# Performance work log

Hardware: AMD Instinct MI355X
Metric: run time of the kernel (lower is better)

The kernel has to match this reference:

```python
import jax, jax.numpy as jnp
import numpy as np

N = 100000      # nodes
E = 1600000     # edges (avg degree 16)
NX = 3          # input feature dim (data.x.shape[1])
K = 2           # number of kernels (len(kernel_DD) = manifold dim)
ORDER = 2       # par['order']
DEPTH = 2       # par['depth']
EPS = 1e-12     # F.normalize eps


def setup_inputs() -> dict:
    key = jax.random.key(0)
    ks = jax.random.split(key, 10)
    x = jax.random.normal(ks[0], (N, NX), dtype=jnp.float32)
    # per-edge kernel weights for the k directional kernels (sparse N x N ops)
    K_DD_vals = 0.1 * jax.random.normal(ks[1], (K, E), dtype=jnp.float32)
    K_DA_vals = 0.1 * jax.random.normal(ks[2], (K, E), dtype=jnp.float32)
    # lin[0]: in = 18*k = 36, out = 72
    lin0_w = 0.05 * jax.random.normal(ks[3], (36, 72), dtype=jnp.float32)
    lin0_b = jnp.zeros((72,), dtype=jnp.float32)
    # MLP: 144 -> 128 -> 64
    mlp_w1 = 0.05 * jax.random.normal(ks[4], (144, 128), dtype=jnp.float32)
    mlp_b1 = jnp.zeros((128,), dtype=jnp.float32)
    mlp_w2 = 0.05 * jax.random.normal(ks[5], (128, 64), dtype=jnp.float32)
    mlp_b2 = jnp.zeros((64,), dtype=jnp.float32)
    src = jax.random.randint(ks[6], (E,), 0, N, dtype=jnp.int32)
    dst = jnp.sort(jax.random.randint(ks[7], (E,), 0, N, dtype=jnp.int32))
    return {"x": x, "K_DD_vals": K_DD_vals, "K_DA_vals": K_DA_vals,
            "lin0_w": lin0_w, "lin0_b": lin0_b,
            "mlp_w1": mlp_w1, "mlp_b1": mlp_b1,
            "mlp_w2": mlp_w2, "mlp_b2": mlp_b2,
            "src": src, "dst": dst}


def _aniso_conv(h, src, dst, k_vals):
    """Kernel-weighted message passing: out_j[t] = sum_{e: dst[e]=t} K_j[e] * h[src[e]].
    Concatenate the k kernel outputs along the channel dim ([N, C] -> [N, k*C])."""
    msgs = h[src]  # [E, C] gather (shared across kernels)
    outs = [jax.ops.segment_sum(k_vals[j][:, None] * msgs, dst, num_segments=N)
            for j in range(k_vals.shape[0])]
    return jnp.concatenate(outs, axis=1)


def reference(x, K_DD_vals, K_DA_vals, lin0_w, lin0_b,
              mlp_w1, mlp_b1, mlp_w2, mlp_b2, src, dst):
    # --- DD phase (order hops), collecting per-hop outputs ---
    h = x
    collected = []
    for _ in range(ORDER):
        h = _aniso_conv(h, src, dst, K_DD_vals)   # channels *= K each hop
        collected.append(h)
    h = jnp.concatenate(collected, axis=1)        # [N, NX*(K + K^2)] = [N, 18]

    # --- DA phase (depth hops) with Linear+ReLU between hops ---
    for i in range(DEPTH):
        h = _aniso_conv(h, src, dst, K_DA_vals)
        if i < DEPTH - 1:
            h = jax.nn.relu(h @ lin0_w + lin0_b)  # 36 -> 72

    # --- MLP head: 144 -> 128 -> 64 ---
    h = jax.nn.relu(h @ mlp_w1 + mlp_b1)
    h = h @ mlp_w2 + mlp_b2

    # --- L2 normalize (F.normalize, p=2, dim=-1) ---
    norm = jnp.maximum(jnp.linalg.norm(h, axis=-1, keepdims=True), EPS)
    return h / norm
```

## Files before the change

kernel.cpp:

```cpp
#include <hip/hip_runtime.h>

#define N_NODES 100000
#define N_EDGES 1600000

typedef __attribute__((ext_vector_type(8))) short short8;
typedef __attribute__((ext_vector_type(4))) float f32x4;
typedef __attribute__((ext_vector_type(2))) unsigned short ushort2v;
typedef __attribute__((ext_vector_type(4))) unsigned short ushort4v;
typedef __attribute__((ext_vector_type(8))) unsigned short ushort8v;

static __device__ inline unsigned short f2bf(float f) {
    union { float f; unsigned u; } v; v.f = f;
    unsigned r = v.u + 0x7FFF + ((v.u >> 16) & 1);
    return (unsigned short)(r >> 16);
}
static __device__ inline float bf2f(unsigned short u) {
    union { unsigned u; float f; } v; v.u = ((unsigned)u) << 16;
    return v.f;
}

__global__ __launch_bounds__(256) void rowptr_k(const int* __restrict__ dst,
                                                int* __restrict__ rp) {
    int t = blockIdx.x * blockDim.x + threadIdx.x;
    if (t > N_NODES) return;
    int lo = 0, hi = N_EDGES;
    while (lo < hi) {
        int mid = (lo + hi) >> 1;
        if (dst[mid] < t) lo = mid + 1; else hi = mid;
    }
    rp[t] = lo;
}

__global__ __launch_bounds__(256) void prep_k(const float* __restrict__ w1,
                                              const float* __restrict__ w2,
                                              const float* __restrict__ l0w,
                                              unsigned short* __restrict__ w1t,
                                              unsigned short* __restrict__ w2t,
                                              unsigned short* __restrict__ w0t) {
    int id = blockIdx.x * blockDim.x + threadIdx.x;
    if (id < 128 * 160) {
        int o = id / 160, k = id - o * 160;
        w1t[id] = (k < 144) ? f2bf(w1[k * 128 + o]) : (unsigned short)0;
    } else if (id < 128 * 160 + 64 * 128) {
        int j = id - 128 * 160;
        int o = j / 128, k = j - o * 128;
        w2t[j] = f2bf(w2[k * 64 + o]);
    } else if (id < 128 * 160 + 64 * 128 + 80 * 64) {
        int j = id - 128 * 160 - 64 * 128;
        int o = j / 64, k = j - o * 64;
        w0t[j] = (o < 72 && k < 36) ? f2bf(l0w[k * 72 + o]) : (unsigned short)0;
    }
}

template<int VEC> struct VecU;
template<> struct VecU<1> { using T = unsigned short; };
template<> struct VecU<2> { using T = ushort2v; };
template<> struct VecU<4> { using T = ushort4v; };
template<> struct VecU<8> { using T = ushort8v; };

template<int OUT_STRIDE>
__global__ __launch_bounds__(256) void conv1_k(const float* __restrict__ hin,
                                               const float* __restrict__ kv,
                                               const int* __restrict__ src,
                                               const int* __restrict__ rp,
                                               unsigned short* __restrict__ hout) {
    int id = blockIdx.x * blockDim.x + threadIdx.x;
    if (id >= N_NODES * 3) return;
    int t = id / 3;
    int c = id - t * 3;
    int e0 = rp[t], e1 = rp[t + 1];
    float a0 = 0.f, a1 = 0.f;
    int e = e0;
    for (; e + 4 <= e1; e += 4) {
        int s[4]; float k0[4], k1[4], v[4];
#pragma unroll
        for (int u = 0; u < 4; ++u) s[u]  = src[e + u];
#pragma unroll
        for (int u = 0; u < 4; ++u) k0[u] = kv[e + u];
#pragma unroll
        for (int u = 0; u < 4; ++u) k1[u] = kv[N_EDGES + e + u];
#pragma unroll
        for (int u = 0; u < 4; ++u) v[u]  = hin[(size_t)s[u] * 3 + c];
#pragma unroll
        for (int u = 0; u < 4; ++u) { a0 += k0[u] * v[u]; a1 += k1[u] * v[u]; }
    }
    for (; e < e1; ++e) {
        int s = src[e];
        float v = hin[(size_t)s * 3 + c];
        a0 += kv[e] * v;
        a1 += kv[N_EDGES + e] * v;
    }
    hout[(size_t)t * OUT_STRIDE + c]     = f2bf(a0);
    hout[(size_t)t * OUT_STRIDE + 3 + c] = f2bf(a1);
}

template<int C, int VEC, int IN_STRIDE, int OUT_STRIDE, int OUT_OFF,
         int PAD_FROM, int PAD_TO>
__global__ __launch_bounds__(256) void convb_k(const unsigned short* __restrict__ hin,
                                               const float* __restrict__ kv,
                                               const int* __restrict__ src,
                                               const int* __restrict__ rp,
                                               unsigned short* __restrict__ hout) {
    constexpr int G = C / VEC;
    using VT = typename VecU<VEC>::T;
    int id = blockIdx.x * blockDim.x + threadIdx.x;
    if (id >= N_NODES * G) return;
    int t = id / G;
    int g = id - t * G;
    int c0 = g * VEC;
    int e0 = rp[t], e1 = rp[t + 1];

    float a0[VEC], a1[VEC];
#pragma unroll
    for (int q = 0; q < VEC; ++q) { a0[q] = 0.f; a1[q] = 0.f; }

    int e = e0;
    for (; e + 4 <= e1; e += 4) {
        int s[4]; float k0[4], k1[4];
#pragma unroll
        for (int u = 0; u < 4; ++u) s[u]  = src[e + u];
#pragma unroll
        for (int u = 0; u < 4; ++u) k0[u] = kv[e + u];
#pragma unroll
        for (int u = 0; u < 4; ++u) k1[u] = kv[N_EDGES + e + u];
        VT v[4];
#pragma unroll
        for (int u = 0; u < 4; ++u)
            v[u] = *reinterpret_cast<const VT*>(hin + (size_t)s[u] * IN_STRIDE + c0);
#pragma unroll
        for (int u = 0; u < 4; ++u) {
            const unsigned short* vf = reinterpret_cast<const unsigned short*>(&v[u]);
#pragma unroll
            for (int q = 0; q < VEC; ++q) {
                float x = bf2f(vf[q]);
                a0[q] += k0[u] * x;
                a1[q] += k1[u] * x;
            }
        }
    }
    for (; e < e1; ++e) {
        int s = src[e];
        float k0 = kv[e], k1 = kv[N_EDGES + e];
        VT v = *reinterpret_cast<const VT*>(hin + (size_t)s * IN_STRIDE + c0);
        const unsigned short* vf = reinterpret_cast<const unsigned short*>(&v);
#pragma unroll
        for (int q = 0; q < VEC; ++q) {
            float x = bf2f(vf[q]);
            a0[q] += k0 * x;
            a1[q] += k1 * x;
        }
    }

    VT r0, r1;
    unsigned short* r0f = reinterpret_cast<unsigned short*>(&r0);
    unsigned short* r1f = reinterpret_cast<unsigned short*>(&r1);
#pragma unroll
    for (int q = 0; q < VEC; ++q) { r0f[q] = f2bf(a0[q]); r1f[q] = f2bf(a1[q]); }
    *reinterpret_cast<VT*>(hout + (size_t)t * OUT_STRIDE + OUT_OFF + c0)     = r0;
    *reinterpret_cast<VT*>(hout + (size_t)t * OUT_STRIDE + OUT_OFF + C + c0) = r1;

    if constexpr (PAD_TO > PAD_FROM) {
        if (g == G - 1) {
            ushort4v z = {0, 0, 0, 0};
#pragma unroll
            for (int j = PAD_FROM; j < PAD_TO; j += 4)
                *reinterpret_cast<ushort4v*>(hout + (size_t)t * OUT_STRIDE + j) = z;
        }
    }
}

__global__ __launch_bounds__(256) void lin0m_k(const unsigned short* __restrict__ h3b,
                                               const unsigned short* __restrict__ w0t,
                                               const float* __restrict__ b0,
                                               unsigned short* __restrict__ h4b) {
    int tid = threadIdx.x;
    int w = tid >> 6;
    int lane = tid & 63;
    int lr = lane & 15;
    int kg = lane >> 4;
    int row_base = blockIdx.x * 64 + w * 16;

    f32x4 acc[5];
#pragma unroll
    for (int n = 0; n < 5; ++n) acc[n] = (f32x4){0.f, 0.f, 0.f, 0.f};

    const unsigned short* arow = h3b + (size_t)(row_base + lr) * 64 + kg * 8;
#pragma unroll
    for (int ks = 0; ks < 2; ++ks) {
        short8 a = *reinterpret_cast<const short8*>(arow + ks * 32);
#pragma unroll
        for (int n = 0; n < 5; ++n) {
            short8 b = *reinterpret_cast<const short8*>(w0t + (n * 16 + lr) * 64 + ks * 32 + kg * 8);
            acc[n] = __builtin_amdgcn_mfma_f32_16x16x32_bf16(a, b, acc[n], 0, 0, 0);
        }
    }
#pragma unroll
    for (int n = 0; n < 5; ++n) {
        int col = n * 16 + lr;
        if (col < 72) {
            float bv = b0[col];
#pragma unroll
            for (int q = 0; q < 4; ++q) {
                int t = row_base + kg * 4 + q;
                if (t < N_NODES)
                    h4b[(size_t)t * 72 + col] = f2bf(fmaxf(acc[n][q] + bv, 0.f));
            }
        }
    }
}

#define HSTRIDE 136
__global__ __launch_bounds__(256) void mlp_k(const unsigned short* __restrict__ h5b,
                                             const unsigned short* __restrict__ w1t,
                                             const float* __restrict__ b1,
                                             const unsigned short* __restrict__ w2t,
                                             const float* __restrict__ b2,
                                             float* __restrict__ out) {
    __shared__ unsigned short sh[64 * HSTRIDE];
    int tid = threadIdx.x;
    int w = tid >> 6;
    int lane = tid & 63;
    int lr = lane & 15;
    int kg = lane >> 4;
    int row_base = blockIdx.x * 64 + w * 16;

    f32x4 acc[8];
#pragma unroll
    for (int n = 0; n < 8; ++n) acc[n] = (f32x4){0.f, 0.f, 0.f, 0.f};

    const unsigned short* arow = h5b + (size_t)(row_base + lr) * 160 + kg * 8;
#pragma unroll
    for (int ks = 0; ks < 5; ++ks) {
        short8 a = *reinterpret_cast<const short8*>(arow + ks * 32);
#pragma unroll
        for (int n = 0; n < 8; ++n) {
            short8 b = *reinterpret_cast<const short8*>(w1t + (n * 16 + lr) * 160 + ks * 32 + kg * 8);
            acc[n] = __builtin_amdgcn_mfma_f32_16x16x32_bf16(a, b, acc[n], 0, 0, 0);
        }
    }
#pragma unroll
    for (int n = 0; n < 8; ++n) {
        float bv = b1[n * 16 + lr];
#pragma unroll
        for (int q = 0; q < 4; ++q) {
            float hv = fmaxf(acc[n][q] + bv, 0.f);
            sh[(w * 16 + kg * 4 + q) * HSTRIDE + n * 16 + lr] = f2bf(hv);
        }
    }
    __syncthreads();

    f32x4 acc2[4];
#pragma unroll
    for (int n = 0; n < 4; ++n) acc2[n] = (f32x4){0.f, 0.f, 0.f, 0.f};
#pragma unroll
    for (int ks = 0; ks < 4; ++ks) {
        short8 a = *reinterpret_cast<const short8*>(sh + (w * 16 + lr) * HSTRIDE + ks * 32 + kg * 8);
#pragma unroll
        for (int n = 0; n < 4; ++n) {
            short8 b = *reinterpret_cast<const short8*>(w2t + (n * 16 + lr) * 128 + ks * 32 + kg * 8);
            acc2[n] = __builtin_amdgcn_mfma_f32_16x16x32_bf16(a, b, acc2[n], 0, 0, 0);
        }
    }

    float v[4][4];
    float ss[4];
#pragma unroll
    for (int q = 0; q < 4; ++q) ss[q] = 0.f;
#pragma unroll
    for (int n = 0; n < 4; ++n) {
        float bv = b2[n * 16 + lr];
#pragma unroll
        for (int q = 0; q < 4; ++q) {
            float x = acc2[n][q] + bv;
            v[n][q] = x;
            ss[q] += x * x;
        }
    }
#pragma unroll
    for (int q = 0; q < 4; ++q) {
#pragma unroll
        for (int d = 1; d < 16; d <<= 1) ss[q] += __shfl_xor(ss[q], d);
    }
#pragma unroll
    for (int q = 0; q < 4; ++q) {
        int node = row_base + kg * 4 + q;
        if (node < N_NODES) {
            float scale = 1.f / fmaxf(sqrtf(ss[q]), 1e-12f);
#pragma unroll
            for (int n = 0; n < 4; ++n)
                out[(size_t)node * 64 + n * 16 + lr] = v[n][q] * scale;
        }
    }
}

extern "C" void kernel_launch(void* const* d_in, const int* in_sizes, int n_in,
                              void* d_out, int out_size, void* d_ws, size_t ws_size,
                              hipStream_t stream) {
    const float* x   = (const float*)d_in[0];
    const float* kdd = (const float*)d_in[1];
    const float* kda = (const float*)d_in[2];
    const float* l0w = (const float*)d_in[3];
    const float* l0b = (const float*)d_in[4];
    const float* w1  = (const float*)d_in[5];
    const float* b1  = (const float*)d_in[6];
    const float* w2  = (const float*)d_in[7];
    const float* b2  = (const float*)d_in[8];
    const int*   src = (const int*)d_in[9];
    const int*   dst = (const int*)d_in[10];
    float* out = (float*)d_out;
    char* ws = (char*)d_ws;

    int*   rp  = (int*)ws;
    unsigned short* w0t = (unsigned short*)(ws + 400384u);
    unsigned short* w1t = (unsigned short*)(ws + 410624u);
    unsigned short* w2t = (unsigned short*)(ws + 451584u);
    unsigned short* hcb = (unsigned short*)(ws + 475136u);
    unsigned short* h3b = (unsigned short*)(ws + 4480000u);
    unsigned short* h4b = (unsigned short*)(ws + 17284096u);
    unsigned short* h5b = (unsigned short*)(ws + 31684096u);

    rowptr_k<<<(N_NODES + 1 + 255) / 256, 256, 0, stream>>>(dst, rp);
    prep_k<<<(128 * 160 + 64 * 128 + 80 * 64 + 255) / 256, 256, 0, stream>>>(w1, w2, l0w, w1t, w2t, w0t);

    conv1_k<20><<<(N_NODES * 3 + 255) / 256, 256, 0, stream>>>(x, kdd, src, rp, hcb);
    convb_k<6, 2, 20, 20, 6, 0, 0><<<(N_NODES * 3 + 255) / 256, 256, 0, stream>>>(hcb, kdd, src, rp, hcb);

    convb_k<18, 2, 20, 64, 0, 36, 64><<<(N_NODES * 9 + 255) / 256, 256, 0, stream>>>(hcb, kda, src, rp, h3b);
    lin0m_k<<<(N_NODES + 63) / 64, 256, 0, stream>>>(h3b, w0t, l0b, h4b);
    convb_k<72, 8, 72, 160, 0, 144, 160><<<(N_NODES * 9 + 255) / 256, 256, 0, stream>>>(h4b, kda, src, rp, h5b);

    mlp_k<<<(N_NODES + 63) / 64, 256, 0, stream>>>(h5b, w1t, b1, w2t, b2, out);
}
```

Before: 197.5 us.

## Fuse last DA conv into MLP head via shared memory; unroll edge loops by 8

```diff
diff --git a/kernel.cpp b/kernel.cpp
--- a/kernel.cpp
+++ b/kernel.cpp
@@ -71,18 +71,18 @@
     int e0 = rp[t], e1 = rp[t + 1];
     float a0 = 0.f, a1 = 0.f;
     int e = e0;
-    for (; e + 4 <= e1; e += 4) {
-        int s[4]; float k0[4], k1[4], v[4];
-#pragma unroll
-        for (int u = 0; u < 4; ++u) s[u]  = src[e + u];
-#pragma unroll
-        for (int u = 0; u < 4; ++u) k0[u] = kv[e + u];
-#pragma unroll
-        for (int u = 0; u < 4; ++u) k1[u] = kv[N_EDGES + e + u];
-#pragma unroll
-        for (int u = 0; u < 4; ++u) v[u]  = hin[(size_t)s[u] * 3 + c];
-#pragma unroll
-        for (int u = 0; u < 4; ++u) { a0 += k0[u] * v[u]; a1 += k1[u] * v[u]; }
+    for (; e + 8 <= e1; e += 8) {
+        int s[8]; float k0[8], k1[8], v[8];
+#pragma unroll
+        for (int u = 0; u < 8; ++u) s[u]  = src[e + u];
+#pragma unroll
+        for (int u = 0; u < 8; ++u) k0[u] = kv[e + u];
+#pragma unroll
+        for (int u = 0; u < 8; ++u) k1[u] = kv[N_EDGES + e + u];
+#pragma unroll
+        for (int u = 0; u < 8; ++u) v[u]  = hin[(size_t)s[u] * 3 + c];
+#pragma unroll
+        for (int u = 0; u < 8; ++u) { a0 += k0[u] * v[u]; a1 += k1[u] * v[u]; }
     }
     for (; e < e1; ++e) {
         int s = src[e];
@@ -115,20 +115,20 @@
     for (int q = 0; q < VEC; ++q) { a0[q] = 0.f; a1[q] = 0.f; }
 
     int e = e0;
-    for (; e + 4 <= e1; e += 4) {
-        int s[4]; float k0[4], k1[4];
-#pragma unroll
-        for (int u = 0; u < 4; ++u) s[u]  = src[e + u];
-#pragma unroll
-        for (int u = 0; u < 4; ++u) k0[u] = kv[e + u];
-#pragma unroll
-        for (int u = 0; u < 4; ++u) k1[u] = kv[N_EDGES + e + u];
-        VT v[4];
-#pragma unroll
-        for (int u = 0; u < 4; ++u)
+    for (; e + 8 <= e1; e += 8) {
+        int s[8]; float k0[8], k1[8];
+#pragma unroll
+        for (int u = 0; u < 8; ++u) s[u]  = src[e + u];
+#pragma unroll
+        for (int u = 0; u < 8; ++u) k0[u] = kv[e + u];
+#pragma unroll
+        for (int u = 0; u < 8; ++u) k1[u] = kv[N_EDGES + e + u];
+        VT v[8];
+#pragma unroll
+        for (int u = 0; u < 8; ++u)
             v[u] = *reinterpret_cast<const VT*>(hin + (size_t)s[u] * IN_STRIDE + c0);
 #pragma unroll
-        for (int u = 0; u < 4; ++u) {
+        for (int u = 0; u < 8; ++u) {
             const unsigned short* vf = reinterpret_cast<const unsigned short*>(&v[u]);
 #pragma unroll
             for (int q = 0; q < VEC; ++q) {
@@ -209,26 +209,93 @@
     }
 }
 
+#define FH 168
 #define HSTRIDE 136
-__global__ __launch_bounds__(256) void mlp_k(const unsigned short* __restrict__ h5b,
-                                             const unsigned short* __restrict__ w1t,
-                                             const float* __restrict__ b1,
-                                             const unsigned short* __restrict__ w2t,
-                                             const float* __restrict__ b2,
-                                             float* __restrict__ out) {
-    __shared__ unsigned short sh[64 * HSTRIDE];
+__global__ __launch_bounds__(256) void fused_k(const unsigned short* __restrict__ h4b,
+                                               const float* __restrict__ kv,
+                                               const int* __restrict__ src,
+                                               const int* __restrict__ rp,
+                                               const unsigned short* __restrict__ w1t,
+                                               const float* __restrict__ b1,
+                                               const unsigned short* __restrict__ w2t,
+                                               const float* __restrict__ b2,
+                                               float* __restrict__ out) {
+    __shared__ unsigned short sh[64 * FH];
+    __shared__ unsigned short shid[64 * HSTRIDE];
     int tid = threadIdx.x;
+    int node0 = blockIdx.x * 64;
+
+    for (int task = tid; task < 576; task += 256) {
+        int nd = task / 9;
+        int g  = task - nd * 9;
+        int t  = node0 + nd;
+        int c0 = g * 8;
+        int e0 = 0, e1 = 0;
+        if (t < N_NODES) { e0 = rp[t]; e1 = rp[t + 1]; }
+
+        float a0[8], a1[8];
+#pragma unroll
+        for (int q = 0; q < 8; ++q) { a0[q] = 0.f; a1[q] = 0.f; }
+
+        int e = e0;
+        for (; e + 8 <= e1; e += 8) {
+            int s[8]; float k0[8], k1[8];
+#pragma unroll
+            for (int u = 0; u < 8; ++u) s[u]  = src[e + u];
+#pragma unroll
+            for (int u = 0; u < 8; ++u) k0[u] = kv[e + u];
+#pragma unroll
+            for (int u = 0; u < 8; ++u) k1[u] = kv[N_EDGES + e + u];
+            ushort8v v[8];
+#pragma unroll
+            for (int u = 0; u < 8; ++u)
+                v[u] = *reinterpret_cast<const ushort8v*>(h4b + (size_t)s[u] * 72 + c0);
+#pragma unroll
+            for (int u = 0; u < 8; ++u) {
+#pragma unroll
+                for (int q = 0; q < 8; ++q) {
+                    float x = bf2f(v[u][q]);
+                    a0[q] += k0[u] * x;
+                    a1[q] += k1[u] * x;
+                }
+            }
+        }
+        for (; e < e1; ++e) {
+            int s = src[e];
+            float k0 = kv[e], k1 = kv[N_EDGES + e];
+            ushort8v v = *reinterpret_cast<const ushort8v*>(h4b + (size_t)s * 72 + c0);
+#pragma unroll
+            for (int q = 0; q < 8; ++q) {
+                float x = bf2f(v[q]);
+                a0[q] += k0 * x;
+                a1[q] += k1 * x;
+            }
+        }
+
+        ushort8v r0, r1;
+#pragma unroll
+        for (int q = 0; q < 8; ++q) { r0[q] = f2bf(a0[q]); r1[q] = f2bf(a1[q]); }
+        *reinterpret_cast<ushort8v*>(sh + nd * FH + c0)      = r0;
+        *reinterpret_cast<ushort8v*>(sh + nd * FH + 72 + c0) = r1;
+    }
+    for (int i = tid; i < 128; i += 256) {
+        int nd = i >> 1, half = i & 1;
+        ushort8v z = {0, 0, 0, 0, 0, 0, 0, 0};
+        *reinterpret_cast<ushort8v*>(sh + nd * FH + 144 + half * 8) = z;
+    }
+    __syncthreads();
+
     int w = tid >> 6;
     int lane = tid & 63;
     int lr = lane & 15;
     int kg = lane >> 4;
-    int row_base = blockIdx.x * 64 + w * 16;
+    int row_base = node0 + w * 16;
 
     f32x4 acc[8];
 #pragma unroll
     for (int n = 0; n < 8; ++n) acc[n] = (f32x4){0.f, 0.f, 0.f, 0.f};
 
-    const unsigned short* arow = h5b + (size_t)(row_base + lr) * 160 + kg * 8;
+    const unsigned short* arow = sh + (w * 16 + lr) * FH + kg * 8;
 #pragma unroll
     for (int ks = 0; ks < 5; ++ks) {
         short8 a = *reinterpret_cast<const short8*>(arow + ks * 32);
@@ -244,7 +311,7 @@
 #pragma unroll
         for (int q = 0; q < 4; ++q) {
             float hv = fmaxf(acc[n][q] + bv, 0.f);
-            sh[(w * 16 + kg * 4 + q) * HSTRIDE + n * 16 + lr] = f2bf(hv);
+            shid[(w * 16 + kg * 4 + q) * HSTRIDE + n * 16 + lr] = f2bf(hv);
         }
     }
     __syncthreads();
@@ -254,7 +321,7 @@
     for (int n = 0; n < 4; ++n) acc2[n] = (f32x4){0.f, 0.f, 0.f, 0.f};
 #pragma unroll
     for (int ks = 0; ks < 4; ++ks) {
-        short8 a = *reinterpret_cast<const short8*>(sh + (w * 16 + lr) * HSTRIDE + ks * 32 + kg * 8);
+        short8 a = *reinterpret_cast<const short8*>(shid + (w * 16 + lr) * HSTRIDE + ks * 32 + kg * 8);
 #pragma unroll
         for (int n = 0; n < 4; ++n) {
             short8 b = *reinterpret_cast<const short8*>(w2t + (n * 16 + lr) * 128 + ks * 32 + kg * 8);
@@ -317,7 +384,6 @@
     unsigned short* hcb = (unsigned short*)(ws + 475136u);
     unsigned short* h3b = (unsigned short*)(ws + 4480000u);
     unsigned short* h4b = (unsigned short*)(ws + 17284096u);
-    unsigned short* h5b = (unsigned short*)(ws + 31684096u);
 
     rowptr_k<<<(N_NODES + 1 + 255) / 256, 256, 0, stream>>>(dst, rp);
     prep_k<<<(128 * 160 + 64 * 128 + 80 * 64 + 255) / 256, 256, 0, stream>>>(w1, w2, l0w, w1t, w2t, w0t);
@@ -327,7 +393,6 @@
 
     convb_k<18, 2, 20, 64, 0, 36, 64><<<(N_NODES * 9 + 255) / 256, 256, 0, stream>>>(hcb, kda, src, rp, h3b);
     lin0m_k<<<(N_NODES + 63) / 64, 256, 0, stream>>>(h3b, w0t, l0b, h4b);
-    convb_k<72, 8, 72, 160, 0, 144, 160><<<(N_NODES * 9 + 255) / 256, 256, 0, stream>>>(h4b, kda, src, rp, h5b);
-
-    mlp_k<<<(N_NODES + 63) / 64, 256, 0, stream>>>(h5b, w1t, b1, w2t, b2, out);
-}
+
+    fused_k<<<(N_NODES + 63) / 64, 256, 0, stream>>>(h4b, kda, src, rp, w1t, b1, w2t, b2, out);
+}
```

After: 206.9 us. +4.8%, slower.
